# Optimization experiments

Hardware: AMD Instinct MI355X
Metric: run time of the kernel (lower is better)

The kernel has to match this reference:

```python
import jax, jax.numpy as jnp
import numpy as np

B, S, D, H = 4, 2048, 1024, 16
HD = D // H
SCALE = HD ** -0.5

def setup_inputs() -> dict:
    key = jax.random.key(0)
    k1, k2, k3 = jax.random.split(key, 3)
    x = jax.random.normal(k1, (B, S, D), dtype=jnp.float32)
    W_qkv = jax.random.normal(k2, (D, 3 * D), dtype=jnp.float32) * (D ** -0.5)
    b_qkv = jnp.zeros((3 * D,), dtype=jnp.float32)
    W_proj = jax.random.normal(k3, (D, D), dtype=jnp.float32) * (D ** -0.5)
    b_proj = jnp.zeros((D,), dtype=jnp.float32)
    return {"x": x, "W_qkv": W_qkv, "b_qkv": b_qkv, "W_proj": W_proj, "b_proj": b_proj}

def reference(x, W_qkv, b_qkv, W_proj, b_proj):
    # x: [B,S,D] -> qkv: [B,S,3D] -> [3,B,H,S,hd]
    qkv = x @ W_qkv + b_qkv
    qkv = qkv.reshape(B, S, 3, H, HD).transpose(2, 0, 3, 1, 4)
    q, k, v = qkv[0], qkv[1], qkv[2]
    # naive full attention: [B,H,S,S]
    attn = jnp.einsum('bhqd,bhkd->bhqk', q, k) * SCALE
    attn = jax.nn.softmax(attn, axis=-1)
    out = jnp.einsum('bhqk,bhkd->bhqd', attn, v)
    out = out.transpose(0, 2, 1, 3).reshape(B, S, D)
    return out @ W_proj + b_proj
```

## Files before the change

kernel.cpp:

```cpp
#include <hip/hip_runtime.h>

typedef __bf16 bf16x8 __attribute__((ext_vector_type(8)));
typedef unsigned short ushort8 __attribute__((ext_vector_type(8)));
typedef float floatx4 __attribute__((ext_vector_type(4)));
typedef unsigned int uintx4 __attribute__((ext_vector_type(4)));

__device__ __forceinline__ unsigned short f2bf(float f) {
  unsigned int u = __builtin_bit_cast(unsigned int, f);
  u += 0x7fffu + ((u >> 16) & 1u);
  return (unsigned short)(u >> 16);
}
__device__ __forceinline__ unsigned int pkbf(float a, float b) {
  unsigned int r;
  asm("v_cvt_pk_bf16_f32 %0, %1, %2" : "=v"(r) : "v"(a), "v"(b));
  return r;
}
__device__ __forceinline__ floatx4 MFMA16(bf16x8 a, bf16x8 b, floatx4 c) {
  return __builtin_amdgcn_mfma_f32_16x16x32_bf16(a, b, c, 0, 0, 0);
}

#define GLOAD16(gsrc, ldst)                                                  \
  __builtin_amdgcn_global_load_lds(                                          \
      (const __attribute__((address_space(1))) void*)(gsrc),                 \
      (__attribute__((address_space(3))) void*)(ldst), 16, 0, 0)

__global__ __launch_bounds__(256) void fill_f32(
    float* __restrict__ out, float val, size_t n) {
  const size_t t = (size_t)blockIdx.x * 256 + threadIdx.x;
  for (size_t i = t; i < n; i += (size_t)gridDim.x * 256) out[i] = val;
}

__global__ __launch_bounds__(256) void cvt_f32_bf16(
    const float* __restrict__ in, unsigned short* __restrict__ out) {
  const size_t t = (size_t)blockIdx.x * 256 + threadIdx.x;
  const float4 a = ((const float4*)in)[2 * t];
  const float4 b = ((const float4*)in)[2 * t + 1];
  uintx4 u;
  u[0] = pkbf(a.x, a.y); u[1] = pkbf(a.z, a.w);
  u[2] = pkbf(b.x, b.y); u[3] = pkbf(b.z, b.w);
  *(uintx4*)&out[t * 8] = u;
}

__global__ __launch_bounds__(256) void transpose_w(
    const float* __restrict__ in, unsigned short* __restrict__ out, int C) {
  __shared__ float T[64][65];
  const int tid = threadIdx.x;
  const int r0 = blockIdx.y * 64, c0 = blockIdx.x * 64;
#pragma unroll
  for (int e = 0; e < 4; ++e) {
    const int idx = e * 256 + tid;
    const int row = idx >> 4, cg = idx & 15;
    const float4 f = *(const float4*)&in[(size_t)(r0 + row) * C + c0 + cg * 4];
    T[row][cg * 4] = f.x; T[row][cg * 4 + 1] = f.y;
    T[row][cg * 4 + 2] = f.z; T[row][cg * 4 + 3] = f.w;
  }
  __syncthreads();
#pragma unroll
  for (int e = 0; e < 2; ++e) {
    const int idx = e * 256 + tid;
    const int cc = idx >> 3, rg = idx & 7;
    uintx4 u;
#pragma unroll
    for (int k = 0; k < 4; ++k)
      u[k] = pkbf(T[rg * 8 + 2 * k][cc], T[rg * 8 + 2 * k + 1][cc]);
    *(uintx4*)&out[(size_t)(c0 + cc) * 1024 + r0 + rg * 8] = u;
  }
}

template <int EPI>
__global__ __launch_bounds__(256) void gemm_nt(
    const unsigned short* __restrict__ A, const unsigned short* __restrict__ Bt,
    const float* __restrict__ bias, unsigned short* __restrict__ o0,
    unsigned short* __restrict__ o1, unsigned short* __restrict__ o2,
    float* __restrict__ of, int M, int N, int K) {
  __shared__ __align__(16) unsigned short As[128 * 32];
  __shared__ __align__(16) unsigned short Bs[128 * 32];
  constexpr int NBX = (EPI == 0) ? 24 : 8;
  constexpr int QX = (NBX * 64) / 8;
  const int tid = threadIdx.x;
  const int lane = tid & 63;
  const int w = tid >> 6;
  const int g = lane >> 4, l15 = lane & 15;
  const int wr = w >> 1, wc = w & 1;
  const int orig = blockIdx.y * NBX + blockIdx.x;
  const int wgid = (orig & 7) * QX + (orig >> 3);
  const int m0 = (wgid / NBX) * 128, n0 = (wgid % NBX) * 128;
  const floatx4 fzero = {0.f, 0.f, 0.f, 0.f};
  floatx4 acc[4][4];
#pragma unroll
  for (int i = 0; i < 4; ++i)
#pragma unroll
    for (int j = 0; j < 4; ++j) acc[i][j] = fzero;

  for (int k0 = 0; k0 < K; k0 += 32) {
#pragma unroll
    for (int p = 0; p < 2; ++p) {
      const int j = p * 256 + tid;
      const int row = j >> 2, cg = j & 3;
      const int dstg = p * 256 + (tid & ~63);
      GLOAD16(&A[(size_t)(m0 + row) * K + k0 + cg * 8], &As[dstg * 8]);
      GLOAD16(&Bt[(size_t)(n0 + row) * K + k0 + cg * 8], &Bs[dstg * 8]);
    }
    __syncthreads();
    bf16x8 af[4], bfr[4];
#pragma unroll
    for (int i = 0; i < 4; ++i)
      af[i] = *(const bf16x8*)&As[(wr * 64 + i * 16 + l15) * 32 + g * 8];
#pragma unroll
    for (int j = 0; j < 4; ++j)
      bfr[j] = *(const bf16x8*)&Bs[(wc * 64 + j * 16 + l15) * 32 + g * 8];
#pragma unroll
    for (int i = 0; i < 4; ++i)
#pragma unroll
      for (int j = 0; j < 4; ++j) acc[i][j] = MFMA16(af[i], bfr[j], acc[i][j]);
    __syncthreads();
  }
#pragma unroll
  for (int i = 0; i < 4; ++i) {
#pragma unroll
    for (int j = 0; j < 4; ++j) {
      const int n = n0 + wc * 64 + j * 16 + l15;
      const float bv = bias[n];
      float vv[4];
#pragma unroll
      for (int r = 0; r < 4; ++r) vv[r] = acc[i][j][r] + bv;
      const int mb = m0 + wr * 64 + i * 16 + g * 4;
      if (EPI == 0) {
        const int three = n >> 10, h = (n >> 6) & 15, hd = n & 63;
        const int b = mb >> 11, s = mb & 2047;
        if (three == 2) {
          ushort4 pk;
          pk.x = f2bf(vv[0]); pk.y = f2bf(vv[1]);
          pk.z = f2bf(vv[2]); pk.w = f2bf(vv[3]);
          const int half = (s >> 5) & 1, hi16 = (s >> 4) & 1, gg = (s >> 2) & 3;
          const int col = (s & ~63) + (half * 4 + gg) * 8 + hi16 * 4;
          *(ushort4*)&o2[(((size_t)(b * 16 + h)) * 64 + hd) * 2048 + col] = pk;
        } else {
          const size_t idx0 = (((size_t)(b * 16 + h)) * 2048 + s) * 64 + hd;
#pragma unroll
          for (int r = 0; r < 4; ++r) {
            if (three == 0)
              o0[idx0 + (size_t)r * 64] = f2bf(vv[r] * 0.1803368801f);
            else
              o1[idx0 + (size_t)r * 64] = f2bf(vv[r]);
          }
        }
      } else {
#pragma unroll
        for (int r = 0; r < 4; ++r) of[(size_t)(mb + r) * N + n] = vv[r];
      }
    }
  }
}

__global__ __launch_bounds__(256) void attn_fwd(
    const unsigned short* __restrict__ Q, const unsigned short* __restrict__ Kq,
    const unsigned short* __restrict__ Vt, unsigned short* __restrict__ Ao) {
  __shared__ __align__(16) unsigned short Ks[2][4096];
  __shared__ __align__(16) unsigned short Vs[2][4096];
  const int bh = blockIdx.y;
  const int tid = threadIdx.x;
  const int lane = tid & 63;
  const int w = tid >> 6;
  const int g = lane >> 4, l15 = lane & 15;
  const int q0 = blockIdx.x * 128 + w * 32;
  const unsigned short* Qp = Q + (size_t)bh * 2048 * 64;
  const unsigned short* Kp = Kq + (size_t)bh * 2048 * 64;
  const unsigned short* Vp = Vt + (size_t)bh * 64 * 2048;

  bf16x8 qf[2][2];
#pragma unroll
  for (int qg = 0; qg < 2; ++qg)
#pragma unroll
    for (int dh = 0; dh < 2; ++dh)
      qf[qg][dh] =
          *(const bf16x8*)&Qp[(size_t)(q0 + qg * 16 + l15) * 64 + dh * 32 + g * 8];

  const floatx4 minit = {-24.f, -24.f, -24.f, -24.f};
  float lpart[2] = {0.0f, 0.0f};
  floatx4 o[2][4];
#pragma unroll
  for (int qg = 0; qg < 2; ++qg)
#pragma unroll
    for (int tl = 0; tl < 4; ++tl) o[qg][tl] = {0.f, 0.f, 0.f, 0.f};

  const int x7 = l15 & 7;
  unsigned koffb[2];
#pragma unroll
  for (int dh = 0; dh < 2; ++dh)
    koffb[dh] = l15 * 128 + (((dh * 4 + g) ^ x7) * 16);
  const char* ksbase = (const char*)&Ks[0][0];
  const char* vsbase = (const char*)&Vs[0][0];

  const unsigned short* ksrc[2];
  const unsigned short* vsrc[2];
  int dsto[2];
#pragma unroll
  for (int p = 0; p < 2; ++p) {
    const int j = p * 256 + tid;
    const int jsrc = (j & ~7) | ((j & 7) ^ ((j >> 3) & 7));
    ksrc[p] = Kp + jsrc * 8;
    const int vrow = j >> 3, sg = j & 7;
    vsrc[p] = Vp + (size_t)vrow * 2048 + (size_t)(sg ^ (vrow & 7)) * 8;
    dsto[p] = (j & ~63) * 8;
  }

#define STAGE(BUF, kv0)                                                       \
  do {                                                                        \
    _Pragma("unroll") for (int p = 0; p < 2; ++p) {                           \
      GLOAD16(ksrc[p] + (size_t)(kv0) * 64, &Ks[BUF][dsto[p]]);               \
      GLOAD16(vsrc[p] + (kv0), &Vs[BUF][dsto[p]]);                            \
    }                                                                         \
  } while (0)

#define CHUNK(BUF, C)                                                         \
  do {                                                                        \
    floatx4 s[2][2];                                                          \
    __builtin_amdgcn_s_setprio(1);                                            \
    _Pragma("unroll") for (int e = 0; e < 2; ++e) {                           \
      const int kvf = (C)*2 + e;                                              \
      bf16x8 kf0 = *(const bf16x8*)(ksbase + (BUF)*8192 + kvf * 2048 +        \
                                    koffb[0]);                                \
      bf16x8 kf1 = *(const bf16x8*)(ksbase + (BUF)*8192 + kvf * 2048 +        \
                                    koffb[1]);                                \
      _Pragma("unroll") for (int qg = 0; qg < 2; ++qg) {                      \
        s[qg][e] = MFMA16(kf0, qf[qg][0], minit);                             \
        s[qg][e] = MFMA16(kf1, qf[qg][1], s[qg][e]);                          \
      }                                                                       \
    }                                                                         \
    __builtin_amdgcn_s_setprio(0);                                            \
    bf16x8 pf[2];                                                             \
    _Pragma("unroll") for (int qg = 0; qg < 2; ++qg) {                        \
      float p0[4], p1[4];                                                     \
      _Pragma("unroll") for (int r = 0; r < 4; ++r) {                         \
        p0[r] = exp2f(s[qg][0][r]);                                           \
        p1[r] = exp2f(s[qg][1][r]);                                           \
      }                                                                       \
      lpart[qg] += ((p0[0] + p0[1]) + (p0[2] + p0[3])) +                      \
                   ((p1[0] + p1[1]) + (p1[2] + p1[3]));                       \
      uintx4 wa;                                                              \
      wa[0] = pkbf(p0[0], p0[1]); wa[1] = pkbf(p0[2], p0[3]);                 \
      wa[2] = pkbf(p1[0], p1[1]); wa[3] = pkbf(p1[2], p1[3]);                 \
      pf[qg] = __builtin_bit_cast(bf16x8, wa);                                \
    }                                                                         \
    __builtin_amdgcn_s_setprio(1);                                            \
    _Pragma("unroll") for (int tl = 0; tl < 4; ++tl) {                        \
      bf16x8 vf = *(const bf16x8*)(vsbase + (BUF)*8192 + tl * 2048 +          \
                                   koffb[(C)]);                               \
      o[0][tl] = MFMA16(pf[0], vf, o[0][tl]);                                 \
      o[1][tl] = MFMA16(pf[1], vf, o[1][tl]);                                 \
    }                                                                         \
    __builtin_amdgcn_s_setprio(0);                                            \
  } while (0)

#define COMPUTE(BUF)                                                          \
  do {                                                                        \
    CHUNK(BUF, 0); CHUNK(BUF, 1);                                             \
  } while (0)

  STAGE(0, 0);
  __syncthreads();
#pragma unroll 1
  for (int t0 = 0; t0 < 32; t0 += 2) {
    STAGE(1, (t0 + 1) * 64);
    COMPUTE(0);
    __syncthreads();
    if (t0 + 2 < 32) STAGE(0, (t0 + 2) * 64);
    COMPUTE(1);
    __syncthreads();
  }
#undef STAGE
#undef CHUNK
#undef COMPUTE

  const int b = bh >> 4, h = bh & 15;
#pragma unroll
  for (int qg = 0; qg < 2; ++qg) {
    float l = lpart[qg];
    l += __shfl_xor(l, 16);
    l += __shfl_xor(l, 32);
    const float linv = 1.0f / l;
    float li[4];
#pragma unroll
    for (int r = 0; r < 4; ++r) li[r] = __shfl(linv, (lane & 48) | (g * 4 + r));
#pragma unroll
    for (int tl = 0; tl < 4; ++tl)
#pragma unroll
      for (int r = 0; r < 4; ++r)
        Ao[((size_t)(b * 2048 + q0 + qg * 16 + g * 4 + r)) * 1024 + h * 64 +
           tl * 16 + l15] = f2bf(o[qg][tl][r] * li[r]);
  }
}

extern "C" void kernel_launch(void* const* d_in, const int* in_sizes, int n_in,
                              void* d_out, int out_size, void* d_ws, size_t ws_size,
                              hipStream_t stream) {
  float* outf = (float*)d_out;
  const size_t OUTN = (size_t)8192 * 1024;

  const float *x = nullptr, *Wqkv = nullptr, *bqkv = nullptr, *Wproj = nullptr,
              *bproj = nullptr;
  for (int i = 0; i < n_in; ++i) {
    switch (in_sizes[i]) {
      case 8388608: x = (const float*)d_in[i]; break;
      case 3145728: Wqkv = (const float*)d_in[i]; break;
      case 3072:    bqkv = (const float*)d_in[i]; break;
      case 1048576: Wproj = (const float*)d_in[i]; break;
      case 1024:    bproj = (const float*)d_in[i]; break;
      default: break;
    }
  }
  if (!x || !Wqkv || !bqkv || !Wproj || !bproj || n_in != 5) {
    fill_f32<<<2048, 256, 0, stream>>>(outf, 5000.0f, OUTN);
    return;
  }
  const size_t SZ = (size_t)4 * 16 * 2048 * 64 * 2;
  if (ws_size < 3 * SZ) {
    fill_f32<<<2048, 256, 0, stream>>>(outf, 1000.0f + (float)(ws_size >> 20), OUTN);
    return;
  }

  char* ws = (char*)d_ws;
  unsigned short* xb = (unsigned short*)(ws);
  unsigned short* Kb = (unsigned short*)(ws + SZ);
  unsigned short* Vtb = (unsigned short*)(ws + 2 * SZ);
  unsigned short* Qb = (unsigned short*)d_out;
  unsigned short* Wtq = (unsigned short*)((char*)d_out + SZ);
  unsigned short* Ao = xb;
  unsigned short* Wtp = Kb;

  cvt_f32_bf16<<<4096, 256, 0, stream>>>(x, xb);
  transpose_w<<<dim3(48, 16), 256, 0, stream>>>(Wqkv, Wtq, 3072);
  gemm_nt<0><<<dim3(24, 64), 256, 0, stream>>>(
      xb, Wtq, bqkv, Qb, Kb, Vtb, nullptr, 8192, 3072, 1024);
  attn_fwd<<<dim3(16, 64), 256, 0, stream>>>(Qb, Kb, Vtb, Ao);
  transpose_w<<<dim3(16, 16), 256, 0, stream>>>(Wproj, Wtp, 1024);
  gemm_nt<1><<<dim3(8, 64), 256, 0, stream>>>(
      Ao, Wtp, bproj, nullptr, nullptr, nullptr, outf, 8192, 1024, 1024);
}
```

Before: 233.2 us.

## Use 512-thread attention blocks with XCD-aware head mapping and merged chunks

Attention blocks grow to 8 waves covering 256 queries, so each K/V tile staged in LDS is shared by twice as many queries and each thread issues a single async load per tile. A 1D grid remaps block indices so that all query tiles of one (batch, head) land on the same XCD, which should improve L2 reuse of K/V. The two per-tile chunks are merged into one compute pass with a wider softmax tree and back-to-back PV MFMAs. In exchange the block is larger and register pressure rises under launch_bounds(512,4), and the grid is halved.

```diff
diff --git a/kernel.cpp b/kernel.cpp
--- a/kernel.cpp
+++ b/kernel.cpp
@@ -153,17 +153,20 @@
   }
 }
 
-__global__ __launch_bounds__(256) void attn_fwd(
+__global__ __launch_bounds__(512, 4) void attn_fwd(
     const unsigned short* __restrict__ Q, const unsigned short* __restrict__ Kq,
     const unsigned short* __restrict__ Vt, unsigned short* __restrict__ Ao) {
   __shared__ __align__(16) unsigned short Ks[2][4096];
   __shared__ __align__(16) unsigned short Vs[2][4096];
-  const int bh = blockIdx.y;
+  const int blk = blockIdx.x;
+  const int xcd = blk & 7, idx = blk >> 3;
+  const int bh = xcd + 8 * (idx >> 3);
+  const int qt = idx & 7;
   const int tid = threadIdx.x;
   const int lane = tid & 63;
   const int w = tid >> 6;
   const int g = lane >> 4, l15 = lane & 15;
-  const int q0 = blockIdx.x * 128 + w * 32;
+  const int q0 = qt * 256 + w * 32;
   const unsigned short* Qp = Q + (size_t)bh * 2048 * 64;
   const unsigned short* Kp = Kq + (size_t)bh * 2048 * 64;
   const unsigned short* Vp = Vt + (size_t)bh * 64 * 2048;
@@ -192,70 +195,65 @@
   const char* ksbase = (const char*)&Ks[0][0];
   const char* vsbase = (const char*)&Vs[0][0];
 
-  const unsigned short* ksrc[2];
-  const unsigned short* vsrc[2];
-  int dsto[2];
-#pragma unroll
-  for (int p = 0; p < 2; ++p) {
-    const int j = p * 256 + tid;
-    const int jsrc = (j & ~7) | ((j & 7) ^ ((j >> 3) & 7));
-    ksrc[p] = Kp + jsrc * 8;
-    const int vrow = j >> 3, sg = j & 7;
-    vsrc[p] = Vp + (size_t)vrow * 2048 + (size_t)(sg ^ (vrow & 7)) * 8;
-    dsto[p] = (j & ~63) * 8;
-  }
+  const int j = tid;
+  const int jsrc = (j & ~7) | ((j & 7) ^ ((j >> 3) & 7));
+  const unsigned short* ksrc = Kp + jsrc * 8;
+  const int vrow = j >> 3, sg = j & 7;
+  const unsigned short* vsrc = Vp + (size_t)vrow * 2048 + (size_t)(sg ^ (vrow & 7)) * 8;
+  const int dsto = (tid & ~63) * 8;
 
 #define STAGE(BUF, kv0)                                                       \
   do {                                                                        \
-    _Pragma("unroll") for (int p = 0; p < 2; ++p) {                           \
-      GLOAD16(ksrc[p] + (size_t)(kv0) * 64, &Ks[BUF][dsto[p]]);               \
-      GLOAD16(vsrc[p] + (kv0), &Vs[BUF][dsto[p]]);                            \
-    }                                                                         \
+    GLOAD16(ksrc + (size_t)(kv0) * 64, &Ks[BUF][dsto]);                       \
+    GLOAD16(vsrc + (kv0), &Vs[BUF][dsto]);                                    \
   } while (0)
 
-#define CHUNK(BUF, C)                                                         \
+#define COMPUTE(BUF)                                                          \
   do {                                                                        \
-    floatx4 s[2][2];                                                          \
+    floatx4 s[2][4];                                                          \
     __builtin_amdgcn_s_setprio(1);                                            \
-    _Pragma("unroll") for (int e = 0; e < 2; ++e) {                           \
-      const int kvf = (C)*2 + e;                                              \
+    _Pragma("unroll") for (int kvf = 0; kvf < 4; ++kvf) {                     \
       bf16x8 kf0 = *(const bf16x8*)(ksbase + (BUF)*8192 + kvf * 2048 +        \
                                     koffb[0]);                                \
       bf16x8 kf1 = *(const bf16x8*)(ksbase + (BUF)*8192 + kvf * 2048 +        \
                                     koffb[1]);                                \
       _Pragma("unroll") for (int qg = 0; qg < 2; ++qg) {                      \
-        s[qg][e] = MFMA16(kf0, qf[qg][0], minit);                             \
-        s[qg][e] = MFMA16(kf1, qf[qg][1], s[qg][e]);                          \
+        s[qg][kvf] = MFMA16(kf0, qf[qg][0], minit);                           \
+        s[qg][kvf] = MFMA16(kf1, qf[qg][1], s[qg][kvf]);                      \
       }                                                                       \
     }                                                                         \
     __builtin_amdgcn_s_setprio(0);                                            \
-    bf16x8 pf[2];                                                             \
+    bf16x8 pf[2][2];                                                          \
     _Pragma("unroll") for (int qg = 0; qg < 2; ++qg) {                        \
-      float p0[4], p1[4];                                                     \
-      _Pragma("unroll") for (int r = 0; r < 4; ++r) {                         \
-        p0[r] = exp2f(s[qg][0][r]);                                           \
-        p1[r] = exp2f(s[qg][1][r]);                                           \
-      }                                                                       \
-      lpart[qg] += ((p0[0] + p0[1]) + (p0[2] + p0[3])) +                      \
-                   ((p1[0] + p1[1]) + (p1[2] + p1[3]));                       \
-      uintx4 wa;                                                              \
-      wa[0] = pkbf(p0[0], p0[1]); wa[1] = pkbf(p0[2], p0[3]);                 \
-      wa[2] = pkbf(p1[0], p1[1]); wa[3] = pkbf(p1[2], p1[3]);                 \
-      pf[qg] = __builtin_bit_cast(bf16x8, wa);                                \
+      float p[4][4];                                                          \
+      _Pragma("unroll") for (int kvf = 0; kvf < 4; ++kvf)                     \
+          _Pragma("unroll") for (int r = 0; r < 4; ++r) p[kvf][r] =           \
+          exp2f(s[qg][kvf][r]);                                               \
+      float t8[8];                                                            \
+      _Pragma("unroll") for (int e = 0; e < 8; ++e) t8[e] =                   \
+          p[e >> 1][(e & 1) * 2] + p[e >> 1][(e & 1) * 2 + 1];                \
+      float t4[4];                                                            \
+      _Pragma("unroll") for (int e = 0; e < 4; ++e) t4[e] =                   \
+          t8[2 * e] + t8[2 * e + 1];                                          \
+      lpart[qg] += (t4[0] + t4[1]) + (t4[2] + t4[3]);                         \
+      uintx4 wa, wb;                                                          \
+      wa[0] = pkbf(p[0][0], p[0][1]); wa[1] = pkbf(p[0][2], p[0][3]);         \
+      wa[2] = pkbf(p[1][0], p[1][1]); wa[3] = pkbf(p[1][2], p[1][3]);         \
+      wb[0] = pkbf(p[2][0], p[2][1]); wb[1] = pkbf(p[2][2], p[2][3]);         \
+      wb[2] = pkbf(p[3][0], p[3][1]); wb[3] = pkbf(p[3][2], p[3][3]);         \
+      pf[qg][0] = __builtin_bit_cast(bf16x8, wa);                             \
+      pf[qg][1] = __builtin_bit_cast(bf16x8, wb);                             \
     }                                                                         \
     __builtin_amdgcn_s_setprio(1);                                            \
     _Pragma("unroll") for (int tl = 0; tl < 4; ++tl) {                        \
-      bf16x8 vf = *(const bf16x8*)(vsbase + (BUF)*8192 + tl * 2048 +          \
-                                   koffb[(C)]);                               \
-      o[0][tl] = MFMA16(pf[0], vf, o[0][tl]);                                 \
-      o[1][tl] = MFMA16(pf[1], vf, o[1][tl]);                                 \
+      _Pragma("unroll") for (int C = 0; C < 2; ++C) {                         \
+        bf16x8 vf = *(const bf16x8*)(vsbase + (BUF)*8192 + tl * 2048 +        \
+                                     koffb[C]);                               \
+        o[0][tl] = MFMA16(pf[0][C], vf, o[0][tl]);                            \
+        o[1][tl] = MFMA16(pf[1][C], vf, o[1][tl]);                            \
+      }                                                                       \
     }                                                                         \
     __builtin_amdgcn_s_setprio(0);                                            \
-  } while (0)
-
-#define COMPUTE(BUF)                                                          \
-  do {                                                                        \
-    CHUNK(BUF, 0); CHUNK(BUF, 1);                                             \
   } while (0)
 
   STAGE(0, 0);
@@ -270,7 +268,6 @@
     __syncthreads();
   }
 #undef STAGE
-#undef CHUNK
 #undef COMPUTE
 
   const int b = bh >> 4, h = bh & 15;
@@ -333,7 +330,7 @@
   transpose_w<<<dim3(48, 16), 256, 0, stream>>>(Wqkv, Wtq, 3072);
   gemm_nt<0><<<dim3(24, 64), 256, 0, stream>>>(
       xb, Wtq, bqkv, Qb, Kb, Vtb, nullptr, 8192, 3072, 1024);
-  attn_fwd<<<dim3(16, 64), 256, 0, stream>>>(Qb, Kb, Vtb, Ao);
+  attn_fwd<<<512, 512, 0, stream>>>(Qb, Kb, Vtb, Ao);
   transpose_w<<<dim3(16, 16), 256, 0, stream>>>(Wproj, Wtp, 1024);
   gemm_nt<1><<<dim3(8, 64), 256, 0, stream>>>(
       Ao, Wtp, bproj, nullptr, nullptr, nullptr, outf, 8192, 1024, 1024);
```

After: 218.4 us. 1.07x faster.
